# Optimization experiments

Measured on AMD Instinct MI355X. Metric: run time of the kernel, lower is better.

## Reference

```python
import jax, jax.numpy as jnp
import numpy as np

N = 65536
R = 9          # num_relations + 1
D_IN = 256
D_HID = 512
D_OUT = 256
N_HIDDEN = 2


def _xavier(key, shape):
    fan_out, fan_in = shape[-2], shape[-1]
    limit = np.sqrt(6.0 / (fan_in + fan_out))
    return jax.random.uniform(key, shape, jnp.float32, -limit, limit)


def setup_inputs() -> dict:
    key = jax.random.key(0)
    ks = jax.random.split(key, 12)
    inp = {
        "x": jax.random.normal(ks[0], (N, D_IN), jnp.float32),
        "edge_attr": jax.random.uniform(ks[1], (N, R), jnp.float32),
    }
    dims = [(D_HID, D_IN)] + [(D_HID, D_HID)] * N_HIDDEN + [(D_OUT, D_HID)]
    for i, (o, ii) in enumerate(dims):
        inp[f"W{i}"] = _xavier(ks[2 + 2 * i], (R, o, ii))
        inp[f"b{i}"] = _xavier(ks[3 + 2 * i], (R, o))
    return inp


def _linear_kg(x, edge_attr, W, b):
    # roi,ni,nr->no : relation-mixed linear per node
    y = jnp.einsum("roi,ni,nr->no", W, x, edge_attr)
    return y + edge_attr @ b


def reference(x, edge_attr, W0, b0, W1, b1, W2, b2, W3, b3):
    y = jax.nn.relu(_linear_kg(x, edge_attr, W0, b0))
    y = jax.nn.relu(_linear_kg(y, edge_attr, W1, b1))
    y = jax.nn.relu(_linear_kg(y, edge_attr, W2, b2))
    y = _linear_kg(y, edge_attr, W3, b3)
    return y
```

## Files before the change

### kernel.cpp

```cpp
#include <hip/hip_runtime.h>
#include <stdint.h>

using f32x4  = __attribute__((ext_vector_type(4))) float;
using bf16x8 = __attribute__((ext_vector_type(8))) __bf16;


__global__ void cvt_x_kernel(const float* __restrict__ x, __bf16* __restrict__ out) {
    const int u    = blockIdx.x * 256 + threadIdx.x;
    const int lane = u & 63;
    const int f    = (u >> 6) & 31;
    const int c    = (u >> 11) & 1;
    const int rb   = u >> 12;
    const int row  = rb * 128 + ((f >> 2) << 4) + (lane & 15);
    const int i    = c * 128 + ((f & 3) << 5) + ((lane >> 4) << 3);
    const float4 a = *(const float4*)(x + (size_t)row * 256 + i);
    const float4 b = *(const float4*)(x + (size_t)row * 256 + i + 4);
    bf16x8 pv;
    pv[0] = (__bf16)a.x; pv[1] = (__bf16)a.y; pv[2] = (__bf16)a.z; pv[3] = (__bf16)a.w;
    pv[4] = (__bf16)b.x; pv[5] = (__bf16)b.y; pv[6] = (__bf16)b.z; pv[7] = (__bf16)b.w;
    *(bf16x8*)(out + (size_t)u * 8) = pv;
}

template<int I, int O>
__global__ void prep_w_kernel(const float* __restrict__ W, __bf16* __restrict__ Bt) {
    constexpr int NCH = I >> 7;
    const int u    = blockIdx.x * 256 + threadIdx.x;
    const int r    = blockIdx.y;
    const int nb   = blockIdx.z;
    const int lane = u & 63;
    const int f    = (u >> 6) & 31;
    const int c    = u >> 11;
    const int row  = nb * 128 + ((f >> 2) << 4) + (lane & 15);
    const int i    = c * 128 + ((f & 3) << 5) + ((lane >> 4) << 3);
    const float* src = W + ((size_t)r * O + row) * I + i;
    const float4 a = *(const float4*)src;
    const float4 b = *(const float4*)(src + 4);
    bf16x8 pv;
    pv[0] = (__bf16)a.x; pv[1] = (__bf16)a.y; pv[2] = (__bf16)a.z; pv[3] = (__bf16)a.w;
    pv[4] = (__bf16)b.x; pv[5] = (__bf16)b.y; pv[6] = (__bf16)b.z; pv[7] = (__bf16)b.w;
    *(bf16x8*)(Bt + (((size_t)nb * 9 + r) * NCH * 2048 + u) * 8) = pv;
}

template<int O>
__global__ void prep_bias_kernel(const float* __restrict__ b, __bf16* __restrict__ BtB) {
    const int u    = blockIdx.x * 256 + threadIdx.x;
    const int nb   = u >> 10;
    const int q    = u & 1023;
    const int lane = q & 63;
    const int f    = q >> 6;
    const int row  = nb * 128 + ((f >> 1) << 4) + (lane & 15);
    const int kb   = ((f & 1) << 5) + ((lane >> 4) << 3);
    bf16x8 pv;
#pragma unroll
    for (int e = 0; e < 8; ++e) {
        const int k = kb + e;
        pv[e] = (k < 9) ? (__bf16)b[(size_t)k * O + row] : (__bf16)0.f;
    }
    *(bf16x8*)(BtB + (size_t)u * 8) = pv;
}

template<int I, int O, bool RELU, bool OUTF32>
__global__ __launch_bounds__(256, 2)
void kg_gemm(const __bf16* __restrict__ A, const float* __restrict__ E,
             const __bf16* __restrict__ Bt, const __bf16* __restrict__ BtB,
             void* __restrict__ Outv) {
    constexpr int NCH = I >> 7;
    constexpr int NBN = O >> 7;
    static_assert((I & 127) == 0 && (O & 127) == 0, "tile divisibility");

    __shared__ __align__(16) char lds[65536 + 4608];
    char*  const ldsA = lds;
    char*  const ldsB = lds + 32768;
    float* const ldsE = (float*)(lds + 65536);

    const int tid  = threadIdx.x;
    const int nwg  = gridDim.x;
    const int braw = blockIdx.x;
    const int bid  = (braw & 7) * (nwg >> 3) + (braw >> 3);
    const int rb   = bid / NBN;
    const int nb   = bid % NBN;
    const int bm0  = rb << 7;
    const int bn0  = nb << 7;
    const int lane = tid & 63;
    const int wid  = tid >> 6;
    const int wr   = (wid >> 1) << 6;
    const int wc   = (wid & 1) << 6;
    const int l15  = lane & 15;
    const int lq   = lane >> 4;

    if (tid < 128) {
        const float* e = E + (size_t)(bm0 + tid) * 9;
#pragma unroll
        for (int q = 0; q < 9; ++q) ldsE[q * 128 + tid] = e[q];
    }

    f32x4 acc[4][4];
#pragma unroll
    for (int m = 0; m < 4; ++m)
#pragma unroll
        for (int n = 0; n < 4; ++n)
            acc[m][n] = f32x4{0.f, 0.f, 0.f, 0.f};
    const f32x4 zero4 = {0.f, 0.f, 0.f, 0.f};

    const size_t Abase = (size_t)rb * NCH * 2048;
    const size_t Bbase = (size_t)nb * 9 * NCH * 2048;

    auto stageTile = [&](char* dst, const __bf16* srcElems) {
#pragma unroll
        for (int rr = 0; rr < 8; ++rr) {
            const int q = rr * 256 + tid;
            __builtin_amdgcn_global_load_lds(
                (const __attribute__((address_space(1))) void*)(srcElems + (size_t)q * 8),
                (__attribute__((address_space(3))) void*)(dst + q * 16), 16, 0, 0);
        }
    };

    const int afb = (wr >> 4) << 2;
    const int bfb = (wc >> 4) << 2;

#pragma unroll 1
    for (int c = 0; c < NCH; ++c) {
        stageTile(ldsA, A + (Abase + (size_t)c * 2048) * 8);
#pragma unroll 1
        for (int r = 0; r < 9; ++r) {
            stageTile(ldsB, Bt + (Bbase + ((size_t)r * NCH + c) * 2048) * 8);
            __syncthreads();
            f32x4 acc2[4][4];
#pragma unroll
            for (int ks = 0; ks < 4; ++ks) {
                bf16x8 av[4], bv[4];
#pragma unroll
                for (int m = 0; m < 4; ++m)
                    av[m] = *(const bf16x8*)(ldsA + (((afb + (m << 2) + ks) << 6) + lane) * 16);
#pragma unroll
                for (int n = 0; n < 4; ++n)
                    bv[n] = *(const bf16x8*)(ldsB + (((bfb + (n << 2) + ks) << 6) + lane) * 16);
#pragma unroll
                for (int m = 0; m < 4; ++m)
#pragma unroll
                    for (int n = 0; n < 4; ++n)
                        acc2[m][n] = __builtin_amdgcn_mfma_f32_16x16x32_bf16(
                            av[m], bv[n], (ks == 0) ? zero4 : acc2[m][n], 0, 0, 0);
            }
#pragma unroll
            for (int m = 0; m < 4; ++m) {
                const f32x4 ev = *(const f32x4*)(ldsE + r * 128 + wr + m * 16 + lq * 4);
#pragma unroll
                for (int n = 0; n < 4; ++n)
#pragma unroll
                    for (int j = 0; j < 4; ++j)
                        acc[m][n][j] += ev[j] * acc2[m][n][j];
            }
            __syncthreads();
        }
    }

    {
#pragma unroll
        for (int rr = 0; rr < 4; ++rr) {
            const int q = rr * 256 + tid;
            __builtin_amdgcn_global_load_lds(
                (const __attribute__((address_space(1))) void*)
                    (BtB + ((size_t)nb * 1024 + q) * 8),
                (__attribute__((address_space(3))) void*)(ldsB + q * 16), 16, 0, 0);
        }
#pragma unroll
        for (int rr = 0; rr < 4; ++rr) {
            const int q    = rr * 256 + tid;
            const int ln   = q & 63;
            const int f    = q >> 6;
            const int row  = ((f >> 1) << 4) + (ln & 15);
            const int kb   = ((f & 1) << 5) + ((ln >> 4) << 3);
            bf16x8 pv;
#pragma unroll
            for (int e8 = 0; e8 < 8; ++e8) {
                const int k = kb + e8;
                pv[e8] = (k < 9) ? (__bf16)ldsE[k * 128 + row] : (__bf16)0.f;
            }
            *(bf16x8*)(ldsA + q * 16) = pv;
        }
        __syncthreads();
#pragma unroll
        for (int ks = 0; ks < 2; ++ks) {
            bf16x8 av[4], bv[4];
#pragma unroll
            for (int m = 0; m < 4; ++m)
                av[m] = *(const bf16x8*)(ldsA + (((((wr >> 4) + m) * 2 + ks) << 6) + lane) * 16);
#pragma unroll
            for (int n = 0; n < 4; ++n)
                bv[n] = *(const bf16x8*)(ldsB + (((((wc >> 4) + n) * 2 + ks) << 6) + lane) * 16);
#pragma unroll
            for (int m = 0; m < 4; ++m)
#pragma unroll
                for (int n = 0; n < 4; ++n)
                    acc[m][n] = __builtin_amdgcn_mfma_f32_16x16x32_bf16(
                        av[m], bv[n], acc[m][n], 0, 0, 0);
        }
    }

    if (OUTF32) {
        const int orow0 = bm0 + wr + lq * 4;
        const int ocol0 = bn0 + wc + l15;
#pragma unroll
        for (int m = 0; m < 4; ++m)
#pragma unroll
            for (int n = 0; n < 4; ++n)
#pragma unroll
                for (int j = 0; j < 4; ++j) {
                    float v = acc[m][n][j];
                    if (RELU) v = fmaxf(v, 0.f);
                    ((float*)Outv)[(size_t)(orow0 + m * 16 + j) * O + (ocol0 + n * 16)] = v;
                }
    } else {
        constexpr int NCHn = O >> 7;
        __bf16* outp = (__bf16*)Outv;
#pragma unroll
        for (int m = 0; m < 4; ++m) {
#pragma unroll
            for (int n = 0; n < 4; ++n) {
                const int col  = bn0 + wc + n * 16 + l15;
                const int c2   = col >> 7;
                const int f2   = (((wr >> 4) + m) << 2) + ((col >> 5) & 3);
                const int ln2  = ((col >> 3) & 3) * 16 + lq * 4;
                const size_t base =
                    (((size_t)rb * NCHn + c2) * 2048 + f2 * 64 + ln2) * 8 + (col & 7);
#pragma unroll
                for (int j = 0; j < 4; ++j) {
                    float v = acc[m][n][j];
                    if (RELU) v = fmaxf(v, 0.f);
                    outp[base + (size_t)j * 8] = (__bf16)v;
                }
            }
        }
    }
}

extern "C" void kernel_launch(void* const* d_in, const int* in_sizes, int n_in,
                              void* d_out, int out_size, void* d_ws, size_t ws_size,
                              hipStream_t stream) {
    const float* x  = (const float*)d_in[0];
    const float* E  = (const float*)d_in[1];
    const float* W0 = (const float*)d_in[2];
    const float* b0 = (const float*)d_in[3];
    const float* W1 = (const float*)d_in[4];
    const float* b1 = (const float*)d_in[5];
    const float* W2 = (const float*)d_in[6];
    const float* b2 = (const float*)d_in[7];
    const float* W3 = (const float*)d_in[8];
    const float* b3 = (const float*)d_in[9];

    char* ws = (char*)d_ws;
    const size_t actBytes = (size_t)65536 * 512 * 2;
    __bf16* actA = (__bf16*)ws;
    __bf16* actB = (__bf16*)(ws + actBytes);
    char* p = ws + 2 * actBytes;
    __bf16* Bt0 = (__bf16*)p; p += (size_t)4 * 9 * 2 * 2048 * 16;
    __bf16* Bt1 = (__bf16*)p; p += (size_t)4 * 9 * 4 * 2048 * 16;
    __bf16* Bt2 = (__bf16*)p; p += (size_t)4 * 9 * 4 * 2048 * 16;
    __bf16* Bt3 = (__bf16*)p; p += (size_t)2 * 9 * 4 * 2048 * 16;
    __bf16* BtB0 = (__bf16*)p; p += (size_t)4 * 1024 * 16;
    __bf16* BtB1 = (__bf16*)p; p += (size_t)4 * 1024 * 16;
    __bf16* BtB2 = (__bf16*)p; p += (size_t)4 * 1024 * 16;
    __bf16* BtB3 = (__bf16*)p; p += (size_t)2 * 1024 * 16;
    if (ws_size < (size_t)(p - ws)) return;

    cvt_x_kernel<<<dim3(8192), dim3(256), 0, stream>>>(x, actA);
    prep_w_kernel<256, 512><<<dim3(16, 9, 4), dim3(256), 0, stream>>>(W0, Bt0);
    prep_w_kernel<512, 512><<<dim3(32, 9, 4), dim3(256), 0, stream>>>(W1, Bt1);
    prep_w_kernel<512, 512><<<dim3(32, 9, 4), dim3(256), 0, stream>>>(W2, Bt2);
    prep_w_kernel<512, 256><<<dim3(32, 9, 2), dim3(256), 0, stream>>>(W3, Bt3);
    prep_bias_kernel<512><<<dim3(16), dim3(256), 0, stream>>>(b0, BtB0);
    prep_bias_kernel<512><<<dim3(16), dim3(256), 0, stream>>>(b1, BtB1);
    prep_bias_kernel<512><<<dim3(16), dim3(256), 0, stream>>>(b2, BtB2);
    prep_bias_kernel<256><<<dim3(8),  dim3(256), 0, stream>>>(b3, BtB3);

    kg_gemm<256, 512, true,  false><<<dim3(2048), dim3(256), 0, stream>>>(actA, E, Bt0, BtB0, actB);
    kg_gemm<512, 512, true,  false><<<dim3(2048), dim3(256), 0, stream>>>(actB, E, Bt1, BtB1, actA);
    kg_gemm<512, 512, true,  false><<<dim3(2048), dim3(256), 0, stream>>>(actA, E, Bt2, BtB2, actB);
    kg_gemm<512, 256, false, true ><<<dim3(1024), dim3(256), 0, stream>>>(actB, E, Bt3, BtB3, d_out);
}
```

Baseline: 919.1 us.

## Split B tiles into halves and prefetch next relation during MFMA compute

Reorders the weight tile layout so each 128-wide B chunk is stored as two K-halves, then double-buffers those halves in LDS. The load of the next relation's half is issued right after the current half's fragments are read into registers, so global-to-LDS traffic overlaps with MFMA work instead of waiting behind a full __syncthreads per relation. Explicit vmcnt/lgkmcnt waits, raw barriers and setprio control the ordering. The manual wait counts are fragile and depend on the exact number of outstanding loads; a miscount would read stale data.

```diff
diff --git a/kernel.cpp b/kernel.cpp
--- a/kernel.cpp
+++ b/kernel.cpp
@@ -3,6 +3,10 @@
 
 using f32x4  = __attribute__((ext_vector_type(4))) float;
 using bf16x8 = __attribute__((ext_vector_type(8))) __bf16;
+
+#define GLOAD_LDS16(src, dst) __builtin_amdgcn_global_load_lds(                 \
+    (const __attribute__((address_space(1))) void*)(src),                      \
+    (__attribute__((address_space(3))) void*)(dst), 16, 0, 0)
 
 
 __global__ void cvt_x_kernel(const float* __restrict__ x, __bf16* __restrict__ out) {
@@ -28,17 +32,20 @@
     const int r    = blockIdx.y;
     const int nb   = blockIdx.z;
     const int lane = u & 63;
-    const int f    = (u >> 6) & 31;
+    const int g    = (u >> 6) & 15;
+    const int h    = (u >> 10) & 1;
     const int c    = u >> 11;
-    const int row  = nb * 128 + ((f >> 2) << 4) + (lane & 15);
-    const int i    = c * 128 + ((f & 3) << 5) + ((lane >> 4) << 3);
+    const int mi   = g >> 1;
+    const int ks   = (h << 1) + (g & 1);
+    const int row  = nb * 128 + mi * 16 + (lane & 15);
+    const int i    = c * 128 + ks * 32 + ((lane >> 4) << 3);
     const float* src = W + ((size_t)r * O + row) * I + i;
     const float4 a = *(const float4*)src;
     const float4 b = *(const float4*)(src + 4);
     bf16x8 pv;
     pv[0] = (__bf16)a.x; pv[1] = (__bf16)a.y; pv[2] = (__bf16)a.z; pv[3] = (__bf16)a.w;
     pv[4] = (__bf16)b.x; pv[5] = (__bf16)b.y; pv[6] = (__bf16)b.z; pv[7] = (__bf16)b.w;
-    *(bf16x8*)(Bt + (((size_t)nb * 9 + r) * NCH * 2048 + u) * 8) = pv;
+    *(bf16x8*)(Bt + ((((size_t)nb * 9 + r) * NCH + c) * 2048 + (u & 2047)) * 8) = pv;
 }
 
 template<int O>
@@ -68,10 +75,11 @@
     constexpr int NBN = O >> 7;
     static_assert((I & 127) == 0 && (O & 127) == 0, "tile divisibility");
 
-    __shared__ __align__(16) char lds[65536 + 4608];
-    char*  const ldsA = lds;
-    char*  const ldsB = lds + 32768;
-    float* const ldsE = (float*)(lds + 65536);
+    __shared__ __align__(16) char lds[32768 + 2 * 16384 + 4608];
+    char*  const ldsA  = lds;
+    char*  const ldsB0 = lds + 32768;
+    char*  const ldsB1 = lds + 49152;
+    float* const ldsE  = (float*)(lds + 65536);
 
     const int tid  = threadIdx.x;
     const int nwg  = gridDim.x;
@@ -104,43 +112,72 @@
 
     const size_t Abase = (size_t)rb * NCH * 2048;
     const size_t Bbase = (size_t)nb * 9 * NCH * 2048;
-
-    auto stageTile = [&](char* dst, const __bf16* srcElems) {
+    const int afb = (wr >> 4) << 2;
+    const int nfb = (wc >> 4) << 1;
+
+    auto stageA = [&](int c) {
+        const __bf16* src = A + (Abase + (size_t)c * 2048) * 8;
 #pragma unroll
         for (int rr = 0; rr < 8; ++rr) {
             const int q = rr * 256 + tid;
-            __builtin_amdgcn_global_load_lds(
-                (const __attribute__((address_space(1))) void*)(srcElems + (size_t)q * 8),
-                (__attribute__((address_space(3))) void*)(dst + q * 16), 16, 0, 0);
+            GLOAD_LDS16(src + (size_t)q * 8, ldsA + q * 16);
         }
     };
-
-    const int afb = (wr >> 4) << 2;
-    const int bfb = (wc >> 4) << 2;
+    auto stageBh = [&](int r, int c, char* dst, int h) {
+        const __bf16* src = Bt + (Bbase + ((size_t)r * NCH + c) * 2048 + (size_t)(h << 10)) * 8;
+#pragma unroll
+        for (int it = 0; it < 4; ++it) {
+            const int q = it * 256 + tid;
+            GLOAD_LDS16(src + (size_t)q * 8, dst + q * 16);
+        }
+    };
 
 #pragma unroll 1
     for (int c = 0; c < NCH; ++c) {
-        stageTile(ldsA, A + (Abase + (size_t)c * 2048) * 8);
+        asm volatile("s_waitcnt lgkmcnt(0)" ::: "memory");
+        __builtin_amdgcn_s_barrier();
+        __builtin_amdgcn_sched_barrier(0);
+        stageA(c);
+        stageBh(0, c, ldsB0, 0);
+        stageBh(0, c, ldsB1, 1);
 #pragma unroll 1
         for (int r = 0; r < 9; ++r) {
-            stageTile(ldsB, Bt + (Bbase + ((size_t)r * NCH + c) * 2048) * 8);
-            __syncthreads();
             f32x4 acc2[4][4];
 #pragma unroll
-            for (int ks = 0; ks < 4; ++ks) {
-                bf16x8 av[4], bv[4];
+            for (int h = 0; h < 2; ++h) {
+                char* const buf = h ? ldsB1 : ldsB0;
+                if (r == 8 && h == 1) asm volatile("s_waitcnt vmcnt(0)" ::: "memory");
+                else                  asm volatile("s_waitcnt vmcnt(4)" ::: "memory");
+                __builtin_amdgcn_s_barrier();
+                __builtin_amdgcn_sched_barrier(0);
+                bf16x8 bv[4][2];
+#pragma unroll
+                for (int n = 0; n < 4; ++n)
+#pragma unroll
+                    for (int j = 0; j < 2; ++j)
+                        bv[n][j] = *(const bf16x8*)(buf + (((nfb + 2 * n + j) << 6) + lane) * 16);
+                asm volatile("s_waitcnt lgkmcnt(0)" ::: "memory");
+                __builtin_amdgcn_sched_barrier(0);
+                __builtin_amdgcn_s_barrier();
+                __builtin_amdgcn_sched_barrier(0);
+                if (r < 8) stageBh(r + 1, c, buf, h);
+                bf16x8 av[4][2];
 #pragma unroll
                 for (int m = 0; m < 4; ++m)
-                    av[m] = *(const bf16x8*)(ldsA + (((afb + (m << 2) + ks) << 6) + lane) * 16);
-#pragma unroll
-                for (int n = 0; n < 4; ++n)
-                    bv[n] = *(const bf16x8*)(ldsB + (((bfb + (n << 2) + ks) << 6) + lane) * 16);
-#pragma unroll
-                for (int m = 0; m < 4; ++m)
-#pragma unroll
-                    for (int n = 0; n < 4; ++n)
-                        acc2[m][n] = __builtin_amdgcn_mfma_f32_16x16x32_bf16(
-                            av[m], bv[n], (ks == 0) ? zero4 : acc2[m][n], 0, 0, 0);
+#pragma unroll
+                    for (int j = 0; j < 2; ++j)
+                        av[m][j] = *(const bf16x8*)(ldsA + (((afb + (m << 2) + 2 * h + j) << 6) + lane) * 16);
+                __builtin_amdgcn_s_setprio(1);
+#pragma unroll
+                for (int j = 0; j < 2; ++j)
+#pragma unroll
+                    for (int m = 0; m < 4; ++m)
+#pragma unroll
+                        for (int n = 0; n < 4; ++n)
+                            acc2[m][n] = __builtin_amdgcn_mfma_f32_16x16x32_bf16(
+                                av[m][j], bv[n][j],
+                                (h == 0 && j == 0) ? zero4 : acc2[m][n], 0, 0, 0);
+                __builtin_amdgcn_s_setprio(0);
             }
 #pragma unroll
             for (int m = 0; m < 4; ++m) {
@@ -151,18 +188,15 @@
                     for (int j = 0; j < 4; ++j)
                         acc[m][n][j] += ev[j] * acc2[m][n][j];
             }
-            __syncthreads();
-        }
-    }
-
+        }
+    }
+
+    __syncthreads();
     {
 #pragma unroll
         for (int rr = 0; rr < 4; ++rr) {
             const int q = rr * 256 + tid;
-            __builtin_amdgcn_global_load_lds(
-                (const __attribute__((address_space(1))) void*)
-                    (BtB + ((size_t)nb * 1024 + q) * 8),
-                (__attribute__((address_space(3))) void*)(ldsB + q * 16), 16, 0, 0);
+            GLOAD_LDS16(BtB + ((size_t)nb * 1024 + q) * 8, ldsB0 + q * 16);
         }
 #pragma unroll
         for (int rr = 0; rr < 4; ++rr) {
@@ -188,7 +222,7 @@
                 av[m] = *(const bf16x8*)(ldsA + (((((wr >> 4) + m) * 2 + ks) << 6) + lane) * 16);
 #pragma unroll
             for (int n = 0; n < 4; ++n)
-                bv[n] = *(const bf16x8*)(ldsB + (((((wc >> 4) + n) * 2 + ks) << 6) + lane) * 16);
+                bv[n] = *(const bf16x8*)(ldsB0 + (((((wc >> 4) + n) * 2 + ks) << 6) + lane) * 16);
 #pragma unroll
             for (int m = 0; m < 4; ++m)
 #pragma unroll
```

Measured after the change: 837.9 us. 8.8% less time.
